# Optimization experiments

Measured on AMD Instinct MI355X. Metric: run time of the kernel, lower is better.

## Reference

```python
import jax, jax.numpy as jnp
import numpy as np

B, NNB, D, FF, L = 128, 510, 128, 512, 3
N = NNB + 2  # 2 query tokens (first/last) + neighbors
SQRT_D = float(np.sqrt(D))
LOGIT_CLIP = 10.0
NINF = -1e9


def _layer_norm(x, g, b):
    m = jnp.mean(x, axis=-1, keepdims=True)
    v = jnp.var(x, axis=-1, keepdims=True)
    return (x - m) * jax.lax.rsqrt(v + 1e-5) * g + b


def _aafm(q, k, v, w):
    # Attention-free module: sigmoid(q) * (exp(w) @ (exp(k)*v)) / (exp(w) @ exp(k))
    w = w - jnp.max(w, axis=-1, keepdims=True)          # stable, cancels in ratio
    k = k - jnp.max(k, axis=1, keepdims=True)
    ew = jnp.exp(w)                                      # [B,N,N]
    ek = jnp.exp(k)                                      # [B,N,D]
    num = jnp.einsum('bts,bsd->btd', ew, ek * v)
    den = jnp.einsum('bts,bsd->btd', ew, ek)
    return jax.nn.sigmoid(q) * num / den


def setup_inputs() -> dict:
    key = jax.random.key(0)
    ks = jax.random.split(key, 32)
    s = 1.0 / np.sqrt(D)
    inp = {
        'lower_xy': jax.random.uniform(ks[0], (B, N, 2), jnp.float32),
        'load': jax.random.uniform(ks[1], (B,), jnp.float32) * 0.9 + 0.1,
        'lower_demand': jax.random.uniform(ks[2], (B, NNB, 1), jnp.float32) * 0.3,
        'lower_cur_ninf_mask': jnp.where(
            jax.random.uniform(ks[3], (B, 1, N)) < 0.1, NINF, 0.0).astype(jnp.float32),
        'lower_pairwise_dist': jax.random.uniform(ks[4], (B, N, N), jnp.float32),
        'neighbors_num_list': jnp.full((B,), NNB, dtype=jnp.int32),
        'lower_neighbors_index': jax.random.randint(ks[5], (B, NNB), 0, 100000),
        # learned params (torch Linear stored transposed: here [in, out], y = x @ W)
        'emb_W': jax.random.normal(ks[6], (2, D)) * s,
        'emb_b': jnp.zeros((D,), jnp.float32),
        'w_load': jax.random.normal(ks[7], (D,)) * s,
        'w_demand': jax.random.normal(ks[8], (D,)) * s,
        'Wq_first': jax.random.normal(ks[9], (D, D)) * s,
        'Wq_last': jax.random.normal(ks[10], (D, D)) * s,
        'alpha_com': jnp.ones((1,), jnp.float32),
        'Wq': jax.random.normal(ks[11], (L, D, D)) * s,
        'Wk': jax.random.normal(ks[12], (L, D, D)) * s,
        'Wv': jax.random.normal(ks[13], (L, D, D)) * s,
        'alpha_attn': jnp.ones((L,), jnp.float32),
        'ln1_g': jnp.ones((L, D), jnp.float32),
        'ln1_b': jnp.zeros((L, D), jnp.float32),
        'ln2_g': jnp.ones((L, D), jnp.float32),
        'ln2_b': jnp.zeros((L, D), jnp.float32),
        'ff_W1': jax.random.normal(ks[14], (L, D, FF)) * s,
        'ff_b1': jnp.zeros((L, FF), jnp.float32),
        'ff_W2': jax.random.normal(ks[15], (L, FF, D)) * (1.0 / np.sqrt(FF)),
        'ff_b2': jnp.zeros((L, D), jnp.float32),
    }
    return inp


def reference(lower_xy, load, lower_demand, lower_cur_ninf_mask, lower_pairwise_dist,
              neighbors_num_list, lower_neighbors_index,
              emb_W, emb_b, w_load, w_demand, Wq_first, Wq_last, alpha_com,
              Wq, Wk, Wv, alpha_attn, ln1_g, ln1_b, ln2_g, ln2_b,
              ff_W1, ff_b1, ff_W2, ff_b2):
    load3 = load[:, None, None]                           # [B,1,1]
    load3 = jnp.where(load3 == 0, 1.0, load3)
    fln = lower_xy @ emb_W + emb_b                        # [B,N,D]
    load_emb = load3 * w_load                             # [B,1,D]
    q_first = fln[:, 0:1] @ Wq_first + load_emb
    q_last = fln[:, 1:2] @ Wq_last + load_emb
    demand = jnp.clip(lower_demand / load3, 0.0, 1.0)     # [B,n,1]
    nb = fln[:, 2:] + demand * w_demand                   # [B,n,D]
    nb_mask = lower_cur_ninf_mask[:, 0, 2:]               # [B,n]
    nb = jnp.where((nb_mask < 0)[..., None], 0.0, nb)     # padding overwrite
    x = jnp.concatenate([q_first, q_last, nb], axis=1)    # [B,N,D]

    log_nb = jnp.log2(neighbors_num_list.astype(x.dtype))[:, None, None]
    spd = -log_nb * lower_pairwise_dist                   # [B,N,N]
    mask_full = jnp.broadcast_to(lower_cur_ninf_mask, spd.shape)

    for i in range(L):
        q = x @ Wq[i]; k = x @ Wk[i]; v = x @ Wv[i]
        aafm = _aafm(q, k, v, alpha_attn[i] * spd + mask_full)
        h = _layer_norm(x + aafm, ln1_g[i], ln1_b[i])
        ff = jax.nn.relu(h @ ff_W1[i] + ff_b1[i]) @ ff_W2[i] + ff_b2[i]
        x = _layer_norm(h + ff, ln2_g[i], ln2_b[i])

    q_out = x[:, 0:1] + x[:, 1:2]                         # [B,1,D]
    nbo = x[:, 2:]                                        # [B,n,D]
    bias_com = alpha_com * spd[:, 1, 2:][:, None, :]      # [B,1,n]
    score = jnp.einsum('bqd,bnd->bqn', q_out, nbo) / SQRT_D + bias_com
    score = LOGIT_CLIP * jnp.tanh(score) + lower_cur_ninf_mask[:, :, 2:]
    probs = jax.nn.softmax(score, axis=-1)[:, 0]          # [B,n]

    selected = jnp.argmax(probs, axis=-1)                 # greedy eval
    prob = jnp.take_along_axis(probs, selected[:, None], axis=-1)[:, 0]
    true_selected = jnp.take_along_axis(lower_neighbors_index, selected[:, None], axis=-1)[:, 0]
    return true_selected, prob
```

## Files before the change

### kernel.cpp

```cpp
#include <hip/hip_runtime.h>
#include <math.h>

constexpr int B   = 128;
constexpr int N   = 512;
constexpr int NNB = 510;
constexpr int D   = 128;
constexpr int FFH = 512;
constexpr int NL  = 3;

__device__ __forceinline__ float sigmoidf_(float x) { return 1.f / (1.f + expf(-x)); }

#define F4ADD(a, b) { (a).x += (b).x; (a).y += (b).y; (a).z += (b).z; (a).w += (b).w; }

__device__ __forceinline__ float xla_fast_tanh(float x) {
    if (fabsf(x) < 0.0004f) return x;
    const float C = 7.99881172180175781f;
    float xc = fminf(fmaxf(x, -C), C);
    float x2 = __fmul_rn(xc, xc);
    float num = -2.76076847742355e-16f;
    num = __builtin_fmaf(x2, num, 2.00018790482477e-13f);
    num = __builtin_fmaf(x2, num, -8.60467152213735e-11f);
    num = __builtin_fmaf(x2, num, 5.12229709037114e-08f);
    num = __builtin_fmaf(x2, num, 1.48572235717979e-05f);
    num = __builtin_fmaf(x2, num, 6.37261928875436e-04f);
    num = __builtin_fmaf(x2, num, 4.89352455891786e-03f);
    num = __fmul_rn(xc, num);
    float den = 1.19825839466702e-06f;
    den = __builtin_fmaf(x2, den, 1.18534705686654e-04f);
    den = __builtin_fmaf(x2, den, 2.26843463243900e-03f);
    den = __builtin_fmaf(x2, den, 4.89352518554385e-03f);
    return num / den;
}

__global__ __launch_bounds__(128) void build_x_kernel(
    const float* __restrict__ xy, const float* __restrict__ load,
    const float* __restrict__ demand, const float* __restrict__ mask,
    const float* __restrict__ embW, const float* __restrict__ embb,
    const float* __restrict__ wload, const float* __restrict__ wdem,
    const float* __restrict__ Wqf, const float* __restrict__ Wql,
    float* __restrict__ x)
{
    __shared__ float fln[128];
    const int bn = blockIdx.x;
    const int b  = bn >> 9;
    const int n  = bn & 511;
    const int d  = threadIdx.x;
    float l = load[b];
    float load3 = (l == 0.f) ? 1.f : l;

    if (n >= 2) {
        const int j = n - 2;
        float m = mask[(size_t)b * N + n];
        float out = 0.f;
        if (!(m < 0.f)) {
            float x0 = xy[(size_t)bn * 2 + 0];
            float x1 = xy[(size_t)bn * 2 + 1];
            float fl = x0 * embW[d] + x1 * embW[D + d] + embb[d];
            float dm = demand[(size_t)b * NNB + j] / load3;
            dm = fminf(fmaxf(dm, 0.f), 1.f);
            out = fl + dm * wdem[d];
        }
        x[(size_t)bn * D + d] = out;
    } else {
        float x0 = xy[(size_t)bn * 2 + 0];
        float x1 = xy[(size_t)bn * 2 + 1];
        fln[d] = x0 * embW[d] + x1 * embW[D + d] + embb[d];
        __syncthreads();
        const float* W = (n == 0) ? Wqf : Wql;
        float acc = 0.f;
        #pragma unroll 8
        for (int e = 0; e < D; ++e) acc = fmaf(fln[e], W[(size_t)e * D + d], acc);
        x[(size_t)bn * D + d] = acc + load3 * wload[d];
    }
}

template<bool BIAS, bool RELU, int LNF>
__global__ __launch_bounds__(256) void gemm_f32(
    const float* __restrict__ A,
    const float* W0, const float* Wb, const float* Wc,
    const float* __restrict__ bias,
    float* C0, float* Cb, float* Cc,
    const float* resid, const float* __restrict__ g, const float* __restrict__ be,
    int M, int K, int Nc)
{
    __shared__ float As[64][40];
    __shared__ float Ws[32][132];
    const float* W = W0;
    float* C = C0;
    int n0 = 0;
    if (Wb != nullptr) {
        if (blockIdx.y == 1)      { W = Wb; C = Cb; }
        else if (blockIdx.y == 2) { W = Wc; C = Cc; }
    } else {
        n0 = blockIdx.y * 128;
    }
    const int m0 = blockIdx.x * 64;
    const int tid = threadIdx.x;
    const int tc = tid & 31;
    const int tr = tid >> 5;

    const int ar0 = tid >> 3,          ac0 = (tid & 7) * 4;
    const int ar1 = (tid + 256) >> 3,  ac1 = ((tid + 256) & 7) * 4;
    int wr[4], wc[4];
    #pragma unroll
    for (int i = 0; i < 4; ++i) {
        int f = tid + i * 256;
        wr[i] = f >> 5; wc[i] = (f & 31) * 4;
    }

    float4 acc[8];
    #pragma unroll
    for (int r = 0; r < 8; ++r) acc[r] = make_float4(0.f, 0.f, 0.f, 0.f);

    {
        float4 a0 = *(const float4*)&A[(size_t)(m0 + ar0) * K + ac0];
        float4 a1 = *(const float4*)&A[(size_t)(m0 + ar1) * K + ac1];
        float4 w0 = *(const float4*)&W[(size_t)(0 + wr[0]) * Nc + n0 + wc[0]];
        float4 w1 = *(const float4*)&W[(size_t)(0 + wr[1]) * Nc + n0 + wc[1]];
        float4 w2 = *(const float4*)&W[(size_t)(0 + wr[2]) * Nc + n0 + wc[2]];
        float4 w3 = *(const float4*)&W[(size_t)(0 + wr[3]) * Nc + n0 + wc[3]];
        *(float4*)&As[ar0][ac0] = a0;
        *(float4*)&As[ar1][ac1] = a1;
        *(float4*)&Ws[wr[0]][wc[0]] = w0;
        *(float4*)&Ws[wr[1]][wc[1]] = w1;
        *(float4*)&Ws[wr[2]][wc[2]] = w2;
        *(float4*)&Ws[wr[3]][wc[3]] = w3;
    }
    __syncthreads();

    for (int kt = 0; kt < K; kt += 32) {
        const bool more = (kt + 32) < K;
        float4 na0, na1, nw0, nw1, nw2, nw3;
        if (more) {
            int kn = kt + 32;
            na0 = *(const float4*)&A[(size_t)(m0 + ar0) * K + kn + ac0];
            na1 = *(const float4*)&A[(size_t)(m0 + ar1) * K + kn + ac1];
            nw0 = *(const float4*)&W[(size_t)(kn + wr[0]) * Nc + n0 + wc[0]];
            nw1 = *(const float4*)&W[(size_t)(kn + wr[1]) * Nc + n0 + wc[1]];
            nw2 = *(const float4*)&W[(size_t)(kn + wr[2]) * Nc + n0 + wc[2]];
            nw3 = *(const float4*)&W[(size_t)(kn + wr[3]) * Nc + n0 + wc[3]];
        }
        #pragma unroll
        for (int kk = 0; kk < 32; kk += 4) {
            float4 w0 = *(float4*)&Ws[kk + 0][tc * 4];
            float4 w1 = *(float4*)&Ws[kk + 1][tc * 4];
            float4 w2 = *(float4*)&Ws[kk + 2][tc * 4];
            float4 w3 = *(float4*)&Ws[kk + 3][tc * 4];
            #pragma unroll
            for (int r = 0; r < 8; ++r) {
                float4 a4 = *(float4*)&As[tr * 8 + r][kk];
                acc[r].x = fmaf(a4.x, w0.x, acc[r].x); acc[r].x = fmaf(a4.y, w1.x, acc[r].x);
                acc[r].x = fmaf(a4.z, w2.x, acc[r].x); acc[r].x = fmaf(a4.w, w3.x, acc[r].x);
                acc[r].y = fmaf(a4.x, w0.y, acc[r].y); acc[r].y = fmaf(a4.y, w1.y, acc[r].y);
                acc[r].y = fmaf(a4.z, w2.y, acc[r].y); acc[r].y = fmaf(a4.w, w3.y, acc[r].y);
                acc[r].z = fmaf(a4.x, w0.z, acc[r].z); acc[r].z = fmaf(a4.y, w1.z, acc[r].z);
                acc[r].z = fmaf(a4.z, w2.z, acc[r].z); acc[r].z = fmaf(a4.w, w3.z, acc[r].z);
                acc[r].w = fmaf(a4.x, w0.w, acc[r].w); acc[r].w = fmaf(a4.y, w1.w, acc[r].w);
                acc[r].w = fmaf(a4.z, w2.w, acc[r].w); acc[r].w = fmaf(a4.w, w3.w, acc[r].w);
            }
        }
        if (more) {
            __syncthreads();
            *(float4*)&As[ar0][ac0] = na0;
            *(float4*)&As[ar1][ac1] = na1;
            *(float4*)&Ws[wr[0]][wc[0]] = nw0;
            *(float4*)&Ws[wr[1]][wc[1]] = nw1;
            *(float4*)&Ws[wr[2]][wc[2]] = nw2;
            *(float4*)&Ws[wr[3]][wc[3]] = nw3;
            __syncthreads();
        }
    }

    float4 bv = make_float4(0.f, 0.f, 0.f, 0.f);
    if (BIAS) bv = *(const float4*)&bias[n0 + tc * 4];
    if constexpr (LNF == 0) {
        #pragma unroll
        for (int r = 0; r < 8; ++r) {
            float4 o = acc[r];
            if (BIAS) { o.x += bv.x; o.y += bv.y; o.z += bv.z; o.w += bv.w; }
            if (RELU) {
                o.x = fmaxf(o.x, 0.f); o.y = fmaxf(o.y, 0.f);
                o.z = fmaxf(o.z, 0.f); o.w = fmaxf(o.w, 0.f);
            }
            *(float4*)&C[(size_t)(m0 + tr * 8 + r) * Nc + n0 + tc * 4] = o;
        }
    } else {
        float4 gv  = *(const float4*)&g[tc * 4];
        float4 bev = *(const float4*)&be[tc * 4];
        #pragma unroll
        for (int r = 0; r < 8; ++r) {
            float4 o = acc[r];
            o.x += bv.x; o.y += bv.y; o.z += bv.z; o.w += bv.w;
            size_t row = (size_t)(m0 + tr * 8 + r);
            float4 xv = *(const float4*)&resid[row * 128 + tc * 4];
            float y0 = xv.x + o.x, y1 = xv.y + o.y, y2 = xv.z + o.z, y3 = xv.w + o.w;
            float s = ((y0 + y1) + y2) + y3;
            #pragma unroll
            for (int mm = 16; mm > 0; mm >>= 1) s += __shfl_xor(s, mm);
            float mean = s * (1.f / 128.f);
            float d0_ = y0 - mean, d1_ = y1 - mean, d2_ = y2 - mean, d3_ = y3 - mean;
            float ss = ((d0_ * d0_ + d1_ * d1_) + d2_ * d2_) + d3_ * d3_;
            #pragma unroll
            for (int mm = 16; mm > 0; mm >>= 1) ss += __shfl_xor(ss, mm);
            float rs = rsqrtf(ss * (1.f / 128.f) + 1e-5f);
            float4 ov;
            ov.x = d0_ * rs * gv.x + bev.x;
            ov.y = d1_ * rs * gv.y + bev.y;
            ov.z = d2_ * rs * gv.z + bev.z;
            ov.w = d3_ * rs * gv.w + bev.w;
            *(float4*)&C[row * 128 + tc * 4] = ov;
        }
    }
}

__global__ __launch_bounds__(128) void colmax_part(
    const float* __restrict__ k, float* __restrict__ part)
{
    int b = blockIdx.x >> 3, c = blockIdx.x & 7, d = threadIdx.x;
    const float* kp = k + ((size_t)b * N + c * 64) * D + d;
    float m = -3.4e38f;
    #pragma unroll 8
    for (int s = 0; s < 64; ++s) m = fmaxf(m, kp[(size_t)s * D]);
    part[(size_t)blockIdx.x * D + d] = m;
}

__global__ __launch_bounds__(128) void ekv_build(
    const float* __restrict__ k, const float* __restrict__ v,
    const float* __restrict__ part, float* __restrict__ ekv)
{
    int b = blockIdx.x >> 3, c = blockIdx.x & 7, d = threadIdx.x;
    float m = -3.4e38f;
    #pragma unroll
    for (int j = 0; j < 8; ++j) m = fmaxf(m, part[((size_t)b * 8 + j) * D + d]);
    for (int s = 0; s < 64; ++s) {
        int sg = c * 64 + s;
        size_t off = ((size_t)b * N + sg) * D + d;
        float ek = expf(k[off] - m);
        size_t o2 = ((size_t)b * N + sg) * 256;
        ekv[o2 + d]       = ek * v[off];
        ekv[o2 + 128 + d] = ek;
    }
}

__global__ __launch_bounds__(256) void attn_kernel(
    const float* __restrict__ pdist, const float* __restrict__ mask,
    const float* __restrict__ ekv, const float* __restrict__ q,
    const float* xres, const float* __restrict__ g, const float* __restrict__ be,
    const int* __restrict__ nnum, const float* __restrict__ alphaAttn, int layer,
    float* outp)
{
    __shared__ float ew[16][516];
    __shared__ float red16[16][16];
    __shared__ float rmax[16];
    const int d0  = blockIdx.x;
    const int xcd = d0 & 7;
    const int idx = d0 >> 3;
    const int tl  = idx & 31;
    const int b   = (idx >> 5) * 8 + xcd;
    const int t0  = tl * 16;
    const int tid = threadIdx.x;
    const float la = -log2f((float)nnum[b]) * alphaAttn[layer];
    const float* pd = pdist + ((size_t)b * N + t0) * N;
    const float* mk = mask + (size_t)b * N;

    #pragma unroll
    for (int i = 0; i < 8; ++i) {
        int f = tid + i * 256;
        int r = f >> 7, s4 = (f & 127) * 4;
        float4 p = *(const float4*)&pd[(size_t)r * N + s4];
        float4 m = *(const float4*)&mk[s4];
        float4 w;
        w.x = fmaf(la, p.x, m.x); w.y = fmaf(la, p.y, m.y);
        w.z = fmaf(la, p.z, m.z); w.w = fmaf(la, p.w, m.w);
        *(float4*)&ew[r][s4] = w;
    }
    __syncthreads();
    {
        int r = tid >> 4, j0 = tid & 15;
        float m = -3.4e38f;
        #pragma unroll 8
        for (int j = 0; j < 32; ++j) m = fmaxf(m, ew[r][j0 + 16 * j]);
        red16[r][j0] = m;
    }
    __syncthreads();
    if (tid < 16) {
        float m = red16[tid][0];
        #pragma unroll
        for (int j = 1; j < 16; ++j) m = fmaxf(m, red16[tid][j]);
        rmax[tid] = m;
    }
    __syncthreads();
    #pragma unroll
    for (int i = 0; i < 8; ++i) {
        int f = tid + i * 256;
        int r = f >> 7, s4 = (f & 127) * 4;
        float m = rmax[r];
        float4 w = *(float4*)&ew[r][s4];
        w.x = expf(w.x - m); w.y = expf(w.y - m);
        w.z = expf(w.z - m); w.w = expf(w.w - m);
        *(float4*)&ew[r][s4] = w;
    }
    __syncthreads();

    const int lane = tid & 63;
    const int wv   = tid >> 6;
    const int c4   = lane * 4;
    float4 acc[16];
    #pragma unroll
    for (int r = 0; r < 16; ++r) acc[r] = make_float4(0.f, 0.f, 0.f, 0.f);
    const float* ep = ekv + (size_t)b * N * 256 + c4;
    const int sb = wv * 128;
    float4 e0 = *(const float4*)&ep[(size_t)(sb + 0) * 256];
    float4 e1 = *(const float4*)&ep[(size_t)(sb + 1) * 256];
    float4 e2 = *(const float4*)&ep[(size_t)(sb + 2) * 256];
    float4 e3 = *(const float4*)&ep[(size_t)(sb + 3) * 256];
    for (int it = 0; it < 32; ++it) {
        const int s = sb + it * 4;
        float4 f0 = e0, f1 = e1, f2 = e2, f3 = e3;
        int sn = (it < 31) ? (s + 4) : s;
        e0 = *(const float4*)&ep[(size_t)(sn + 0) * 256];
        e1 = *(const float4*)&ep[(size_t)(sn + 1) * 256];
        e2 = *(const float4*)&ep[(size_t)(sn + 2) * 256];
        e3 = *(const float4*)&ep[(size_t)(sn + 3) * 256];
        #pragma unroll
        for (int r = 0; r < 16; ++r) {
            float4 a = *(float4*)&ew[r][s];
            acc[r].x = fmaf(a.x, f0.x, acc[r].x); acc[r].x = fmaf(a.y, f1.x, acc[r].x);
            acc[r].x = fmaf(a.z, f2.x, acc[r].x); acc[r].x = fmaf(a.w, f3.x, acc[r].x);
            acc[r].y = fmaf(a.x, f0.y, acc[r].y); acc[r].y = fmaf(a.y, f1.y, acc[r].y);
            acc[r].y = fmaf(a.z, f2.y, acc[r].y); acc[r].y = fmaf(a.w, f3.y, acc[r].y);
            acc[r].z = fmaf(a.x, f0.z, acc[r].z); acc[r].z = fmaf(a.y, f1.z, acc[r].z);
            acc[r].z = fmaf(a.z, f2.z, acc[r].z); acc[r].z = fmaf(a.w, f3.z, acc[r].z);
            acc[r].w = fmaf(a.x, f0.w, acc[r].w); acc[r].w = fmaf(a.y, f1.w, acc[r].w);
            acc[r].w = fmaf(a.z, f2.w, acc[r].w); acc[r].w = fmaf(a.w, f3.w, acc[r].w);
        }
    }

    float* red = &ew[0][0];
    __syncthreads();
    if (wv == 1) {
        #pragma unroll
        for (int r = 0; r < 16; ++r) *(float4*)&red[r * 256 + c4] = acc[r];
    }
    if (wv == 3) {
        #pragma unroll
        for (int r = 0; r < 16; ++r) *(float4*)&red[4096 + r * 256 + c4] = acc[r];
    }
    __syncthreads();
    if (wv == 0) {
        #pragma unroll
        for (int r = 0; r < 16; ++r) { float4 t = *(float4*)&red[r * 256 + c4]; F4ADD(acc[r], t); }
    }
    if (wv == 2) {
        #pragma unroll
        for (int r = 0; r < 16; ++r) { float4 t = *(float4*)&red[4096 + r * 256 + c4]; F4ADD(acc[r], t); }
    }
    __syncthreads();
    if (wv == 2) {
        #pragma unroll
        for (int r = 0; r < 16; ++r) *(float4*)&red[r * 256 + c4] = acc[r];
    }
    __syncthreads();
    if (wv == 0) {
        #pragma unroll
        for (int r = 0; r < 16; ++r) {
            float4 t = *(float4*)&red[r * 256 + c4];
            F4ADD(acc[r], t);
            *(float4*)&red[r * 256 + c4] = acc[r];
        }
    }
    __syncthreads();

    if (lane < 32) {
        const int c = lane * 4;
        #pragma unroll
        for (int i = 0; i < 4; ++i) {
            int row = wv * 4 + i;
            float4 nu = *(float4*)&red[row * 256 + c];
            float4 de = *(float4*)&red[row * 256 + 128 + c];
            size_t off = ((size_t)b * N + t0 + row) * D + c;
            float4 qq = *(const float4*)&q[off];
            float4 av;
            av.x = sigmoidf_(qq.x) * nu.x / de.x;
            av.y = sigmoidf_(qq.y) * nu.y / de.y;
            av.z = sigmoidf_(qq.z) * nu.z / de.z;
            av.w = sigmoidf_(qq.w) * nu.w / de.w;
            float4 xv = *(const float4*)&xres[off];
            float y0 = xv.x + av.x, y1 = xv.y + av.y;
            float y2 = xv.z + av.z, y3 = xv.w + av.w;
            float s = ((y0 + y1) + y2) + y3;
            #pragma unroll
            for (int mm = 16; mm > 0; mm >>= 1) s += __shfl_xor(s, mm);
            float mean = s * (1.f / 128.f);
            float d0_ = y0 - mean, d1_ = y1 - mean, d2_ = y2 - mean, d3_ = y3 - mean;
            float ss = ((d0_ * d0_ + d1_ * d1_) + d2_ * d2_) + d3_ * d3_;
            #pragma unroll
            for (int mm = 16; mm > 0; mm >>= 1) ss += __shfl_xor(ss, mm);
            float rs = rsqrtf(ss * (1.f / 128.f) + 1e-5f);
            float4 ov;
            ov.x = d0_ * rs * g[c]     + be[c];
            ov.y = d1_ * rs * g[c + 1] + be[c + 1];
            ov.z = d2_ * rs * g[c + 2] + be[c + 2];
            ov.w = d3_ * rs * g[c + 3] + be[c + 3];
            *(float4*)&outp[off] = ov;
        }
    }
}

__global__ __launch_bounds__(512) void k_final(
    const float* __restrict__ x, const float* __restrict__ pdist,
    const float* __restrict__ mask, const int* __restrict__ nnum,
    const int* __restrict__ nidx, const float* __restrict__ aCom,
    float* __restrict__ out)
{
    __shared__ float  sc[512];
    __shared__ float  ee[512];
    __shared__ double qo[128];
    int b = blockIdx.x, tid = threadIdx.x;
    const float* xb = x + (size_t)b * N * D;
    if (tid < 128) qo[tid] = (double)xb[tid] + (double)xb[128 + tid];
    __syncthreads();
    if (tid < NNB) {
        const float* xr = xb + (size_t)(2 + tid) * 128;
        double s = 0.0;
        for (int dd = 0; dd < 128; ++dd) s += qo[dd] * (double)xr[dd];
        double lg = -log2((double)nnum[b]);
        s = s / 11.313708498984761
          + (double)aCom[0] * lg * (double)pdist[((size_t)b * 512 + 1) * 512 + 2 + tid];
        float t = xla_fast_tanh((float)s);
        sc[tid] = __fadd_rn(__fmul_rn(10.0f, t),
                            mask[(size_t)b * 512 + 2 + tid]);
    }
    __syncthreads();
    if (tid == 0) {
        float m = -3.4e38f;
        for (int n2 = 0; n2 < NNB; ++n2) m = fmaxf(m, sc[n2]);
        float S = 0.f;
        for (int n2 = 0; n2 < NNB; ++n2) {
            float e = expf(__fadd_rn(sc[n2], -m));
            ee[n2] = e;
            S = __fadd_rn(S, e);
        }
        float bestp = -1.f; int sel = 0;
        for (int n2 = 0; n2 < NNB; ++n2) {
            float p = ee[n2] / S;
            if (p > bestp) { bestp = p; sel = n2; }
        }
        out[b]     = (float)nidx[(size_t)b * NNB + sel];
        out[B + b] = bestp;
    }
}

extern "C" void kernel_launch(void* const* d_in, const int* in_sizes, int n_in,
                              void* d_out, int out_size, void* d_ws, size_t ws_size,
                              hipStream_t stream)
{
    const float* xy     = (const float*)d_in[0];
    const float* load   = (const float*)d_in[1];
    const float* demand = (const float*)d_in[2];
    const float* mask   = (const float*)d_in[3];
    const float* pdist  = (const float*)d_in[4];
    const int*   nnum   = (const int*)d_in[5];
    const int*   nidx   = (const int*)d_in[6];
    const float* embW   = (const float*)d_in[7];
    const float* embb   = (const float*)d_in[8];
    const float* wload  = (const float*)d_in[9];
    const float* wdem   = (const float*)d_in[10];
    const float* Wqf    = (const float*)d_in[11];
    const float* Wql    = (const float*)d_in[12];
    const float* aCom   = (const float*)d_in[13];
    const float* Wq     = (const float*)d_in[14];
    const float* Wk     = (const float*)d_in[15];
    const float* Wv     = (const float*)d_in[16];
    const float* aAttn  = (const float*)d_in[17];
    const float* ln1g   = (const float*)d_in[18];
    const float* ln1b   = (const float*)d_in[19];
    const float* ln2g   = (const float*)d_in[20];
    const float* ln2b   = (const float*)d_in[21];
    const float* fW1    = (const float*)d_in[22];
    const float* fb1    = (const float*)d_in[23];
    const float* fW2    = (const float*)d_in[24];
    const float* fb2    = (const float*)d_in[25];
    float* out = (float*)d_out;

    float* ws = (float*)d_ws;
    const size_t SZ = (size_t)B * N * D;
    float* xbuf  = ws;
    float* qbuf  = ws + SZ;
    float* kbuf  = ws + 2 * SZ;
    float* vbuf  = ws + 3 * SZ;
    float* ekv   = ws + 4 * SZ;
    float* part  = ws + 6 * SZ;
    float* bigh  = kbuf;

    build_x_kernel<<<B * N, 128, 0, stream>>>(xy, load, demand, mask, embW, embb,
                                              wload, wdem, Wqf, Wql, xbuf);
    const int M = B * N;
    for (int l = 0; l < NL; ++l) {
        gemm_f32<false, false, 0><<<dim3(M / 64, 3), 256, 0, stream>>>(
            xbuf, Wq + (size_t)l * D * D, Wk + (size_t)l * D * D, Wv + (size_t)l * D * D,
            nullptr, qbuf, kbuf, vbuf, nullptr, nullptr, nullptr, M, D, D);
        colmax_part<<<B * 8, 128, 0, stream>>>(kbuf, part);
        ekv_build<<<B * 8, 128, 0, stream>>>(kbuf, vbuf, part, ekv);
        attn_kernel<<<B * 32, 256, 0, stream>>>(
            pdist, mask, ekv, qbuf, xbuf, ln1g + l * D, ln1b + l * D,
            nnum, aAttn, l, xbuf);
        gemm_f32<true, true, 0><<<dim3(M / 64, FFH / 128), 256, 0, stream>>>(
            xbuf, fW1 + (size_t)l * D * FFH, nullptr, nullptr, fb1 + l * FFH,
            bigh, nullptr, nullptr, nullptr, nullptr, nullptr, M, D, FFH);
        gemm_f32<true, false, 1><<<dim3(M / 64, 1), 256, 0, stream>>>(
            bigh, fW2 + (size_t)l * FFH * D, nullptr, nullptr, fb2 + l * D,
            xbuf, nullptr, nullptr, xbuf, ln2g + l * D, ln2b + l * D, M, FFH, D);
    }
    k_final<<<B, 512, 0, stream>>>(xbuf, pdist, mask, nnum, nidx, aCom, out);
}
```

Measured before the change: 1.821 ms.

## Enlarge GEMM per-thread register tile to 8x8 with 128-thread blocks

The FP32 GEMM now gives each thread an 8x8 output tile instead of 8x4 and halves the block size to 128 threads, with each thread loading more of the A and W tiles. This raises FMA work per LDS read of A and cuts shared-memory traffic per flop. The fused LayerNorm epilogue is adapted to 16 threads per row. The cost is more registers per thread and fewer waves available to hide latency.

```diff
diff --git a/kernel.cpp b/kernel.cpp
--- a/kernel.cpp
+++ b/kernel.cpp
@@ -75,7 +75,7 @@
 }
 
 template<bool BIAS, bool RELU, int LNF>
-__global__ __launch_bounds__(256) void gemm_f32(
+__global__ __launch_bounds__(128) void gemm_f32(
     const float* __restrict__ A,
     const float* W0, const float* Wb, const float* Wc,
     const float* __restrict__ bias,
@@ -95,120 +95,158 @@
         n0 = blockIdx.y * 128;
     }
     const int m0 = blockIdx.x * 64;
-    const int tid = threadIdx.x;
-    const int tc = tid & 31;
-    const int tr = tid >> 5;
-
-    const int ar0 = tid >> 3,          ac0 = (tid & 7) * 4;
-    const int ar1 = (tid + 256) >> 3,  ac1 = ((tid + 256) & 7) * 4;
-    int wr[4], wc[4];
+    const int tid  = threadIdx.x;
+    const int rowg = tid >> 4;
+    const int colg = tid & 15;
+    const int c8   = colg * 8;
+
+    int ar[4], ac[4];
     #pragma unroll
     for (int i = 0; i < 4; ++i) {
-        int f = tid + i * 256;
+        int f = tid + i * 128;
+        ar[i] = f >> 3; ac[i] = (f & 7) * 4;
+    }
+    int wr[8], wc[8];
+    #pragma unroll
+    for (int i = 0; i < 8; ++i) {
+        int f = tid + i * 128;
         wr[i] = f >> 5; wc[i] = (f & 31) * 4;
     }
 
-    float4 acc[8];
-    #pragma unroll
-    for (int r = 0; r < 8; ++r) acc[r] = make_float4(0.f, 0.f, 0.f, 0.f);
+    float4 acc[8][2];
+    #pragma unroll
+    for (int r = 0; r < 8; ++r) {
+        acc[r][0] = make_float4(0.f, 0.f, 0.f, 0.f);
+        acc[r][1] = make_float4(0.f, 0.f, 0.f, 0.f);
+    }
 
     {
-        float4 a0 = *(const float4*)&A[(size_t)(m0 + ar0) * K + ac0];
-        float4 a1 = *(const float4*)&A[(size_t)(m0 + ar1) * K + ac1];
-        float4 w0 = *(const float4*)&W[(size_t)(0 + wr[0]) * Nc + n0 + wc[0]];
-        float4 w1 = *(const float4*)&W[(size_t)(0 + wr[1]) * Nc + n0 + wc[1]];
-        float4 w2 = *(const float4*)&W[(size_t)(0 + wr[2]) * Nc + n0 + wc[2]];
-        float4 w3 = *(const float4*)&W[(size_t)(0 + wr[3]) * Nc + n0 + wc[3]];
-        *(float4*)&As[ar0][ac0] = a0;
-        *(float4*)&As[ar1][ac1] = a1;
-        *(float4*)&Ws[wr[0]][wc[0]] = w0;
-        *(float4*)&Ws[wr[1]][wc[1]] = w1;
-        *(float4*)&Ws[wr[2]][wc[2]] = w2;
-        *(float4*)&Ws[wr[3]][wc[3]] = w3;
+        float4 av[4], wv[8];
+        #pragma unroll
+        for (int i = 0; i < 4; ++i)
+            av[i] = *(const float4*)&A[(size_t)(m0 + ar[i]) * K + ac[i]];
+        #pragma unroll
+        for (int i = 0; i < 8; ++i)
+            wv[i] = *(const float4*)&W[(size_t)wr[i] * Nc + n0 + wc[i]];
+        #pragma unroll
+        for (int i = 0; i < 4; ++i) *(float4*)&As[ar[i]][ac[i]] = av[i];
+        #pragma unroll
+        for (int i = 0; i < 8; ++i) *(float4*)&Ws[wr[i]][wc[i]] = wv[i];
     }
     __syncthreads();
 
     for (int kt = 0; kt < K; kt += 32) {
         const bool more = (kt + 32) < K;
-        float4 na0, na1, nw0, nw1, nw2, nw3;
+        float4 nav[4], nwv[8];
         if (more) {
             int kn = kt + 32;
-            na0 = *(const float4*)&A[(size_t)(m0 + ar0) * K + kn + ac0];
-            na1 = *(const float4*)&A[(size_t)(m0 + ar1) * K + kn + ac1];
-            nw0 = *(const float4*)&W[(size_t)(kn + wr[0]) * Nc + n0 + wc[0]];
-            nw1 = *(const float4*)&W[(size_t)(kn + wr[1]) * Nc + n0 + wc[1]];
-            nw2 = *(const float4*)&W[(size_t)(kn + wr[2]) * Nc + n0 + wc[2]];
-            nw3 = *(const float4*)&W[(size_t)(kn + wr[3]) * Nc + n0 + wc[3]];
+            #pragma unroll
+            for (int i = 0; i < 4; ++i)
+                nav[i] = *(const float4*)&A[(size_t)(m0 + ar[i]) * K + kn + ac[i]];
+            #pragma unroll
+            for (int i = 0; i < 8; ++i)
+                nwv[i] = *(const float4*)&W[(size_t)(kn + wr[i]) * Nc + n0 + wc[i]];
         }
         #pragma unroll
         for (int kk = 0; kk < 32; kk += 4) {
-            float4 w0 = *(float4*)&Ws[kk + 0][tc * 4];
-            float4 w1 = *(float4*)&Ws[kk + 1][tc * 4];
-            float4 w2 = *(float4*)&Ws[kk + 2][tc * 4];
-            float4 w3 = *(float4*)&Ws[kk + 3][tc * 4];
+            float4 w00 = *(float4*)&Ws[kk + 0][c8];
+            float4 w01 = *(float4*)&Ws[kk + 0][c8 + 4];
+            float4 w10 = *(float4*)&Ws[kk + 1][c8];
+            float4 w11 = *(float4*)&Ws[kk + 1][c8 + 4];
+            float4 w20 = *(float4*)&Ws[kk + 2][c8];
+            float4 w21 = *(float4*)&Ws[kk + 2][c8 + 4];
+            float4 w30 = *(float4*)&Ws[kk + 3][c8];
+            float4 w31 = *(float4*)&Ws[kk + 3][c8 + 4];
             #pragma unroll
             for (int r = 0; r < 8; ++r) {
-                float4 a4 = *(float4*)&As[tr * 8 + r][kk];
-                acc[r].x = fmaf(a4.x, w0.x, acc[r].x); acc[r].x = fmaf(a4.y, w1.x, acc[r].x);
-                acc[r].x = fmaf(a4.z, w2.x, acc[r].x); acc[r].x = fmaf(a4.w, w3.x, acc[r].x);
-                acc[r].y = fmaf(a4.x, w0.y, acc[r].y); acc[r].y = fmaf(a4.y, w1.y, acc[r].y);
-                acc[r].y = fmaf(a4.z, w2.y, acc[r].y); acc[r].y = fmaf(a4.w, w3.y, acc[r].y);
-                acc[r].z = fmaf(a4.x, w0.z, acc[r].z); acc[r].z = fmaf(a4.y, w1.z, acc[r].z);
-                acc[r].z = fmaf(a4.z, w2.z, acc[r].z); acc[r].z = fmaf(a4.w, w3.z, acc[r].z);
-                acc[r].w = fmaf(a4.x, w0.w, acc[r].w); acc[r].w = fmaf(a4.y, w1.w, acc[r].w);
-                acc[r].w = fmaf(a4.z, w2.w, acc[r].w); acc[r].w = fmaf(a4.w, w3.w, acc[r].w);
+                float4 a4 = *(float4*)&As[rowg * 8 + r][kk];
+                acc[r][0].x = fmaf(a4.x, w00.x, acc[r][0].x); acc[r][0].x = fmaf(a4.y, w10.x, acc[r][0].x);
+                acc[r][0].x = fmaf(a4.z, w20.x, acc[r][0].x); acc[r][0].x = fmaf(a4.w, w30.x, acc[r][0].x);
+                acc[r][0].y = fmaf(a4.x, w00.y, acc[r][0].y); acc[r][0].y = fmaf(a4.y, w10.y, acc[r][0].y);
+                acc[r][0].y = fmaf(a4.z, w20.y, acc[r][0].y); acc[r][0].y = fmaf(a4.w, w30.y, acc[r][0].y);
+                acc[r][0].z = fmaf(a4.x, w00.z, acc[r][0].z); acc[r][0].z = fmaf(a4.y, w10.z, acc[r][0].z);
+                acc[r][0].z = fmaf(a4.z, w20.z, acc[r][0].z); acc[r][0].z = fmaf(a4.w, w30.z, acc[r][0].z);
+                acc[r][0].w = fmaf(a4.x, w00.w, acc[r][0].w); acc[r][0].w = fmaf(a4.y, w10.w, acc[r][0].w);
+                acc[r][0].w = fmaf(a4.z, w20.w, acc[r][0].w); acc[r][0].w = fmaf(a4.w, w30.w, acc[r][0].w);
+                acc[r][1].x = fmaf(a4.x, w01.x, acc[r][1].x); acc[r][1].x = fmaf(a4.y, w11.x, acc[r][1].x);
+                acc[r][1].x = fmaf(a4.z, w21.x, acc[r][1].x); acc[r][1].x = fmaf(a4.w, w31.x, acc[r][1].x);
+                acc[r][1].y = fmaf(a4.x, w01.y, acc[r][1].y); acc[r][1].y = fmaf(a4.y, w11.y, acc[r][1].y);
+                acc[r][1].y = fmaf(a4.z, w21.y, acc[r][1].y); acc[r][1].y = fmaf(a4.w, w31.y, acc[r][1].y);
+                acc[r][1].z = fmaf(a4.x, w01.z, acc[r][1].z); acc[r][1].z = fmaf(a4.y, w11.z, acc[r][1].z);
+                acc[r][1].z = fmaf(a4.z, w21.z, acc[r][1].z); acc[r][1].z = fmaf(a4.w, w31.z, acc[r][1].z);
+                acc[r][1].w = fmaf(a4.x, w01.w, acc[r][1].w); acc[r][1].w = fmaf(a4.y, w11.w, acc[r][1].w);
+                acc[r][1].w = fmaf(a4.z, w21.w, acc[r][1].w); acc[r][1].w = fmaf(a4.w, w31.w, acc[r][1].w);
             }
         }
         if (more) {
             __syncthreads();
-            *(float4*)&As[ar0][ac0] = na0;
-            *(float4*)&As[ar1][ac1] = na1;
-            *(float4*)&Ws[wr[0]][wc[0]] = nw0;
-            *(float4*)&Ws[wr[1]][wc[1]] = nw1;
-            *(float4*)&Ws[wr[2]][wc[2]] = nw2;
-            *(float4*)&Ws[wr[3]][wc[3]] = nw3;
+            #pragma unroll
+            for (int i = 0; i < 4; ++i) *(float4*)&As[ar[i]][ac[i]] = nav[i];
+            #pragma unroll
+            for (int i = 0; i < 8; ++i) *(float4*)&Ws[wr[i]][wc[i]] = nwv[i];
             __syncthreads();
         }
     }
 
-    float4 bv = make_float4(0.f, 0.f, 0.f, 0.f);
-    if (BIAS) bv = *(const float4*)&bias[n0 + tc * 4];
+    float4 bv0 = make_float4(0.f, 0.f, 0.f, 0.f), bv1 = bv0;
+    if (BIAS) {
+        bv0 = *(const float4*)&bias[n0 + c8];
+        bv1 = *(const float4*)&bias[n0 + c8 + 4];
+    }
     if constexpr (LNF == 0) {
         #pragma unroll
         for (int r = 0; r < 8; ++r) {
-            float4 o = acc[r];
-            if (BIAS) { o.x += bv.x; o.y += bv.y; o.z += bv.z; o.w += bv.w; }
+            float4 o0 = acc[r][0], o1 = acc[r][1];
+            if (BIAS) { F4ADD(o0, bv0); F4ADD(o1, bv1); }
             if (RELU) {
-                o.x = fmaxf(o.x, 0.f); o.y = fmaxf(o.y, 0.f);
-                o.z = fmaxf(o.z, 0.f); o.w = fmaxf(o.w, 0.f);
+                o0.x = fmaxf(o0.x, 0.f); o0.y = fmaxf(o0.y, 0.f);
+                o0.z = fmaxf(o0.z, 0.f); o0.w = fmaxf(o0.w, 0.f);
+                o1.x = fmaxf(o1.x, 0.f); o1.y = fmaxf(o1.y, 0.f);
+                o1.z = fmaxf(o1.z, 0.f); o1.w = fmaxf(o1.w, 0.f);
             }
-            *(float4*)&C[(size_t)(m0 + tr * 8 + r) * Nc + n0 + tc * 4] = o;
+            size_t base = (size_t)(m0 + rowg * 8 + r) * Nc + n0 + c8;
+            *(float4*)&C[base]     = o0;
+            *(float4*)&C[base + 4] = o1;
         }
     } else {
-        float4 gv  = *(const float4*)&g[tc * 4];
-        float4 bev = *(const float4*)&be[tc * 4];
+        float4 gv0  = *(const float4*)&g[c8];
+        float4 gv1  = *(const float4*)&g[c8 + 4];
+        float4 bev0 = *(const float4*)&be[c8];
+        float4 bev1 = *(const float4*)&be[c8 + 4];
         #pragma unroll
         for (int r = 0; r < 8; ++r) {
-            float4 o = acc[r];
-            o.x += bv.x; o.y += bv.y; o.z += bv.z; o.w += bv.w;
-            size_t row = (size_t)(m0 + tr * 8 + r);
-            float4 xv = *(const float4*)&resid[row * 128 + tc * 4];
-            float y0 = xv.x + o.x, y1 = xv.y + o.y, y2 = xv.z + o.z, y3 = xv.w + o.w;
-            float s = ((y0 + y1) + y2) + y3;
-            #pragma unroll
-            for (int mm = 16; mm > 0; mm >>= 1) s += __shfl_xor(s, mm);
+            float4 o0 = acc[r][0], o1 = acc[r][1];
+            F4ADD(o0, bv0); F4ADD(o1, bv1);
+            size_t row = (size_t)(m0 + rowg * 8 + r);
+            float4 xv0 = *(const float4*)&resid[row * 128 + c8];
+            float4 xv1 = *(const float4*)&resid[row * 128 + c8 + 4];
+            float y0 = xv0.x + o0.x, y1 = xv0.y + o0.y, y2 = xv0.z + o0.z, y3 = xv0.w + o0.w;
+            float y4 = xv1.x + o1.x, y5 = xv1.y + o1.y, y6 = xv1.z + o1.z, y7 = xv1.w + o1.w;
+            float sA = ((y0 + y1) + y2) + y3;
+            float sB = ((y4 + y5) + y6) + y7;
+            float s = sA + sB;
+            #pragma unroll
+            for (int mm = 8; mm > 0; mm >>= 1) s += __shfl_xor(s, mm);
             float mean = s * (1.f / 128.f);
             float d0_ = y0 - mean, d1_ = y1 - mean, d2_ = y2 - mean, d3_ = y3 - mean;
-            float ss = ((d0_ * d0_ + d1_ * d1_) + d2_ * d2_) + d3_ * d3_;
-            #pragma unroll
-            for (int mm = 16; mm > 0; mm >>= 1) ss += __shfl_xor(ss, mm);
+            float d4_ = y4 - mean, d5_ = y5 - mean, d6_ = y6 - mean, d7_ = y7 - mean;
+            float vA = ((d0_ * d0_ + d1_ * d1_) + d2_ * d2_) + d3_ * d3_;
+            float vB = ((d4_ * d4_ + d5_ * d5_) + d6_ * d6_) + d7_ * d7_;
+            float ss = vA + vB;
+            #pragma unroll
+            for (int mm = 8; mm > 0; mm >>= 1) ss += __shfl_xor(ss, mm);
             float rs = rsqrtf(ss * (1.f / 128.f) + 1e-5f);
-            float4 ov;
-            ov.x = d0_ * rs * gv.x + bev.x;
-            ov.y = d1_ * rs * gv.y + bev.y;
-            ov.z = d2_ * rs * gv.z + bev.z;
-            ov.w = d3_ * rs * gv.w + bev.w;
-            *(float4*)&C[row * 128 + tc * 4] = ov;
+            float4 ov0, ov1;
+            ov0.x = d0_ * rs * gv0.x + bev0.x;
+            ov0.y = d1_ * rs * gv0.y + bev0.y;
+            ov0.z = d2_ * rs * gv0.z + bev0.z;
+            ov0.w = d3_ * rs * gv0.w + bev0.w;
+            ov1.x = d4_ * rs * gv1.x + bev1.x;
+            ov1.y = d5_ * rs * gv1.y + bev1.y;
+            ov1.z = d6_ * rs * gv1.z + bev1.z;
+            ov1.w = d7_ * rs * gv1.w + bev1.w;
+            *(float4*)&C[row * 128 + c8]     = ov0;
+            *(float4*)&C[row * 128 + c8 + 4] = ov1;
         }
     }
 }
@@ -497,7 +535,7 @@
                                               wload, wdem, Wqf, Wql, xbuf);
     const int M = B * N;
     for (int l = 0; l < NL; ++l) {
-        gemm_f32<false, false, 0><<<dim3(M / 64, 3), 256, 0, stream>>>(
+        gemm_f32<false, false, 0><<<dim3(M / 64, 3), 128, 0, stream>>>(
             xbuf, Wq + (size_t)l * D * D, Wk + (size_t)l * D * D, Wv + (size_t)l * D * D,
             nullptr, qbuf, kbuf, vbuf, nullptr, nullptr, nullptr, M, D, D);
         colmax_part<<<B * 8, 128, 0, stream>>>(kbuf, part);
@@ -505,10 +543,10 @@
         attn_kernel<<<B * 32, 256, 0, stream>>>(
             pdist, mask, ekv, qbuf, xbuf, ln1g + l * D, ln1b + l * D,
             nnum, aAttn, l, xbuf);
-        gemm_f32<true, true, 0><<<dim3(M / 64, FFH / 128), 256, 0, stream>>>(
+        gemm_f32<true, true, 0><<<dim3(M / 64, FFH / 128), 128, 0, stream>>>(
             xbuf, fW1 + (size_t)l * D * FFH, nullptr, nullptr, fb1 + l * FFH,
             bigh, nullptr, nullptr, nullptr, nullptr, nullptr, M, D, FFH);
-        gemm_f32<true, false, 1><<<dim3(M / 64, 1), 256, 0, stream>>>(
+        gemm_f32<true, false, 1><<<dim3(M / 64, 1), 128, 0, stream>>>(
             bigh, fW2 + (size_t)l * FFH * D, nullptr, nullptr, fb2 + l * D,
             xbuf, nullptr, nullptr, xbuf, ln2g + l * D, ln2b + l * D, M, FFH, D);
     }
```

Result: slower. 2.363 ms (+29.7%).
